# Kernel optimization log

Measured on AMD Instinct MI355X. Metric: run time of the kernel, lower is better.

The kernel has to match this reference:

```python
import jax, jax.numpy as jnp
from jax import lax
import numpy as np

B, S, T, R = 64, 50, 50, 2   # batch, n_prev_sents, n_words, n_responses
V, H = 32000, 256            # vocab, hidden (= emb_size)


def gru_scan(xs, h0, Wih, Whh, bih, bhh):
    """Torch-style GRU over xs [T, N, I]; returns (outs [T,N,H], h_last [N,H])."""
    gi_all = jnp.einsum('tni,gi->tng', xs, Wih) + bih  # input gates precomputed
    def step(h, gi):
        gh = h @ Whh.T + bhh
        ir, iz, inn = jnp.split(gi, 3, -1)
        hr, hz, hn = jnp.split(gh, 3, -1)
        r = jax.nn.sigmoid(ir + hr)
        z = jax.nn.sigmoid(iz + hz)
        n = jnp.tanh(inn + r * hn)
        h = (1.0 - z) * n + z * h
        return h, h
    h_last, outs = lax.scan(step, h0, gi_all)
    return outs, h_last


def agent_tables():
    # replicates get_agent_emb: np.random.seed(1), one fresh uniform table per batch
    np.random.seed(1)
    return jnp.asarray(np.stack([np.random.uniform(0, 1, (S + 1, H)) for _ in range(B)]).astype(np.float32))


def setup_inputs() -> dict:
    key = jax.random.key(0)
    ks = jax.random.split(key, 24)
    k = 1.0 / np.sqrt(H)
    u = lambda kk, shape: jax.random.uniform(kk, shape, jnp.float32, -k, k)
    inp = {
        'context': jax.random.randint(ks[0], (B, S, T), 0, V, jnp.int32),
        'response': jax.random.randint(ks[1], (B, R, T), 0, V, jnp.int32),
        'spk_agents': jax.random.randint(ks[2], (B, S), 0, S + 1, jnp.int32),
        'emb_utter': jax.random.normal(ks[3], (V, H), jnp.float32) * 0.1,
        'emb_resp': jax.random.normal(ks[4], (V, H), jnp.float32) * 0.1,
        'utter_Wih': u(ks[5], (3 * H, H)), 'utter_Whh': u(ks[6], (3 * H, H)),
        'utter_bih': u(ks[7], (3 * H,)), 'utter_bhh': u(ks[8], (3 * H,)),
        'ctx_Wih': u(ks[9], (3 * H, 2 * H)), 'ctx_Whh': u(ks[10], (3 * H, H)),
        'ctx_bih': u(ks[11], (3 * H,)), 'ctx_bhh': u(ks[12], (3 * H,)),
        'resp_Wih': u(ks[13], (3 * H, H)), 'resp_Whh': u(ks[14], (3 * H, H)),
        'resp_bih': u(ks[15], (3 * H,)), 'resp_bhh': u(ks[16], (3 * H,)),
        'spk_Wih': u(ks[17], (3 * H, H)), 'spk_Whh': u(ks[18], (3 * H, H)),
        'spk_bih': u(ks[19], (3 * H,)), 'spk_bhh': u(ks[20], (3 * H,)),
    }
    return inp


def forward(context, response, spk_agents, emb_utter, emb_resp,
            utter_Wih, utter_Whh, utter_bih, utter_bhh,
            ctx_Wih, ctx_Whh, ctx_bih, ctx_bhh,
            resp_Wih, resp_Whh, resp_bih, resp_bhh,
            spk_Wih, spk_Whh, spk_bih, spk_bhh):
    # ---- utterance encoder: all B*S utterances batched through one GRU ----
    xu = emb_utter[context.reshape(B * S, T)]                 # [B*S, T, H]
    xu = jnp.transpose(xu, (1, 0, 2))                         # [T, B*S, H]
    _, hu = gru_scan(xu, jnp.zeros((B * S, H), jnp.float32),
                     utter_Wih, utter_Whh, utter_bih, utter_bhh)
    utter_hidden = hu.reshape(B, S, H).transpose(1, 0, 2)     # [S, B, H]

    # ---- agent embeddings (per-batch random tables, gathered by speaker id) ----
    tables = agent_tables()                                   # [B, S+1, H] constant
    agent_emb = jnp.take_along_axis(tables, spk_agents[:, :, None].astype(jnp.int32), axis=1)  # [B,S,H]
    agent_emb = jnp.transpose(agent_emb, (1, 0, 2))           # [S, B, H]

    # ---- context GRU over utterances ----
    ctx_in = jnp.concatenate([utter_hidden, agent_emb], axis=2)  # [S, B, 2H]
    context_output, ctx_h = gru_scan(ctx_in, jnp.zeros((B, H), jnp.float32),
                                     ctx_Wih, ctx_Whh, ctx_bih, ctx_bhh)
    context_hidden = ctx_h[None]                              # [1, B, H]

    # ---- speaker encoder: masked GRU == GRU over each speaker's subsequence ----
    sp_ids = jnp.arange(S + 1)
    active = (spk_agents[:, :, None] == sp_ids[None, None, :])  # [B, S, S+1]
    active_t = jnp.transpose(active, (1, 0, 2))                 # [S, B, S+1]
    gi_all = jnp.einsum('sbh,gh->sbg', context_output, spk_Wih) + spk_bih  # [S, B, 3H]

    def spk_step(h, inputs):
        gi, act = inputs                                        # gi [B,3H], act [B,S+1]
        gh = jnp.einsum('bsh,gh->bsg', h, spk_Whh) + spk_bhh    # [B, S+1, 3H]
        ir, iz, inn = jnp.split(gi[:, None, :], 3, -1)
        hr, hz, hn = jnp.split(gh, 3, -1)
        r = jax.nn.sigmoid(ir + hr)
        z = jax.nn.sigmoid(iz + hz)
        n = jnp.tanh(inn + r * hn)
        h_new = (1.0 - z) * n + z * h
        return jnp.where(act[:, :, None], h_new, h), None

    h_spk, _ = lax.scan(spk_step, jnp.zeros((B, S + 1, H), jnp.float32), (gi_all, active_t))
    present = active.any(axis=1)                               # [B, S+1]
    spk_emb = h_spk * present[:, :, None]                      # rows of absent speakers stay 0
    spk_emb_mask = (present & (sp_ids[None, :] > 0)).astype(jnp.float32)  # [B, S+1]

    # ---- response encoder: all B*R responses batched ----
    xr = emb_resp[response.reshape(B * R, T)]                  # [B*R, T, H]
    xr = jnp.transpose(xr, (1, 0, 2))                          # [T, B*R, H]
    outs, hr_ = gru_scan(xr, jnp.zeros((B * R, H), jnp.float32),
                         resp_Wih, resp_Whh, resp_bih, resp_bhh)
    resp_output = outs.reshape(T, B, R, H).transpose(2, 0, 1, 3)  # [R, T, B, H]
    resp_hidden = hr_.reshape(B, R, H).transpose(1, 0, 2)         # [R, B, H]

    return (context_output, context_hidden, resp_output, resp_hidden, spk_emb, spk_emb_mask)


def reference(context, response, spk_agents, emb_utter, emb_resp,
              utter_Wih, utter_Whh, utter_bih, utter_bhh,
              ctx_Wih, ctx_Whh, ctx_bih, ctx_bhh,
              resp_Wih, resp_Whh, resp_bih, resp_bhh,
              spk_Wih, spk_Whh, spk_bih, spk_bhh):
    return forward(context, response, spk_agents, emb_utter, emb_resp,
                   utter_Wih, utter_Whh, utter_bih, utter_bhh,
                   ctx_Wih, ctx_Whh, ctx_bih, ctx_bhh,
                   resp_Wih, resp_Whh, resp_bih, resp_bhh,
                   spk_Wih, spk_Whh, spk_bih, spk_bhh)
```

## Files before the change

kernel.cpp:

```cpp
#include <hip/hip_runtime.h>
#include <hip/hip_bf16.h>
#include <stdint.h>
#include <stdlib.h>
#include <math.h>

typedef __hip_bfloat16 bf16;
typedef unsigned short ushort;
typedef __attribute__((ext_vector_type(8))) short bhalf8;
typedef __attribute__((ext_vector_type(4))) float f32x4;

#define Bn 64
#define Sn 50
#define Tn 50
#define Hn 256

#define OFF_CTX_OUT   0
#define OFF_CTX_HID   819200
#define OFF_RESP_OUT  835584
#define OFF_RESP_HID  2473984
#define OFF_SPK_EMB   2506752
#define OFF_SPK_MASK  3342336

#define WS_FLAG   0u
#define WS_HU     256u
#define WS_REG    1638912u
#define RG_UTTQ   0u
#define RG_UTTSC  24576000u
#define RG_RESPGI 0u
#define RG_CO     9830400u
#define RG_GIC    13107200u
#define RG_GIS    18022400u
#define RG_TBL    22937600u
#define WS_END    26342912u

__device__ __forceinline__ float b2f_bits(unsigned int b) {
    union { unsigned int u; float f; } c; c.u = b; return c.f;
}
__device__ __forceinline__ float bf2f(ushort v) { return b2f_bits(((unsigned int)v) << 16); }
__device__ __forceinline__ ushort f2bf(float f) {
    union { float f; unsigned int u; } c; c.f = f;
    return (ushort)((c.u + 0x7fffu + ((c.u >> 16) & 1u)) >> 16);
}
__device__ __forceinline__ void gld_lds16(const void* g, void* l) {
    __builtin_amdgcn_global_load_lds(
        (const __attribute__((address_space(1))) void*)g,
        (__attribute__((address_space(3))) void*)l, 16, 0, 0);
}
template<bool BF>
__device__ __forceinline__ bhalf8 ldfrag(const void* __restrict__ p, size_t i) {
    if (BF) {
        return *(const bhalf8*)((const ushort*)p + i);
    } else {
        const float* q = (const float*)p + i;
        float4 a = *(const float4*)q;
        float4 b = *(const float4*)(q + 4);
        bhalf8 r;
        r[0] = (short)f2bf(a.x); r[1] = (short)f2bf(a.y);
        r[2] = (short)f2bf(a.z); r[3] = (short)f2bf(a.w);
        r[4] = (short)f2bf(b.x); r[5] = (short)f2bf(b.y);
        r[6] = (short)f2bf(b.z); r[7] = (short)f2bf(b.w);
        return r;
    }
}
template<bool BF>
__device__ __forceinline__ float ldw(const void* __restrict__ p, int i) {
    return BF ? bf2f(((const ushort*)p)[i]) : ((const float*)p)[i];
}
template<bool BF>
__device__ __forceinline__ void stout(void* __restrict__ out, size_t i, float v) {
    if (BF) ((ushort*)out)[i] = f2bf(v);
    else    ((float*)out)[i] = v;
}
__device__ __forceinline__ float fsigm(float x) {
    return __builtin_amdgcn_rcpf(1.f + __expf(-x));
}
__device__ __forceinline__ float ftanh(float x) {
    float e = __expf(-2.f * x);
    return (1.f - e) * __builtin_amdgcn_rcpf(1.f + e);
}

__global__ void sniff_kernel(const void* __restrict__ w, int* __restrict__ flag) {
    const unsigned int* p = (const unsigned int*)w;
    int tid = threadIdx.x;
    bool big = false;
    for (int i = tid; i < 512; i += 64) {
        float v = b2f_bits(p[i] << 16);
        if (!(fabsf(v) <= 1.0f)) big = true;
    }
    unsigned long long m = __ballot(big);
    if (tid == 0) *flag = (m == 0ull) ? 1 : 0;
}


template<bool BF>
__device__ void vocab_utt_body(
    const void* __restrict__ emb_u, const void* __restrict__ uWih,
    const void* __restrict__ ubih,
    char* __restrict__ Q, float* __restrict__ SC,
    float* bhs, float (*rmx)[16])
{
    const int tid = threadIdx.x;
    const int w = tid >> 6, l = tid & 63, quad = l >> 4, c = l & 15;

    for (int i = tid; i < 768; i += 512) bhs[i] = ldw<BF>(ubih, i);

    bhalf8 wf[3][2][8];
    #pragma unroll
    for (int g = 0; g < 3; ++g)
        #pragma unroll
        for (int ctl = 0; ctl < 2; ++ctl) {
            const int gcol = g * 256 + 32 * w + 16 * ctl + c;
            #pragma unroll
            for (int tk = 0; tk < 8; ++tk)
                wf[g][ctl][tk] = ldfrag<BF>(uWih, (size_t)gcol * 256 + 32 * tk + 8 * quad);
        }
    __syncthreads();

    for (int vt = blockIdx.x; vt < 2000; vt += gridDim.x) {
        f32x4 acc[3][2];
        #pragma unroll
        for (int g = 0; g < 3; ++g)
            #pragma unroll
            for (int ctl = 0; ctl < 2; ++ctl) {
                float b = bhs[g * 256 + 32 * w + 16 * ctl + c];
                acc[g][ctl] = (f32x4){b, b, b, b};
            }
        #pragma unroll
        for (int tk = 0; tk < 8; ++tk) {
            bhalf8 a = ldfrag<BF>(emb_u, (size_t)(vt * 16 + c) * 256 + 32 * tk + 8 * quad);
            #pragma unroll
            for (int g = 0; g < 3; ++g)
                #pragma unroll
                for (int ctl = 0; ctl < 2; ++ctl)
                    acc[g][ctl] = __builtin_amdgcn_mfma_f32_16x16x32_bf16(
                        a, wf[g][ctl][tk], acc[g][ctl], 0, 0, 0);
        }

        float mx[4];
        #pragma unroll
        for (int r = 0; r < 4; ++r) {
            float v = 0.f;
            #pragma unroll
            for (int g = 0; g < 3; ++g)
                #pragma unroll
                for (int ctl = 0; ctl < 2; ++ctl)
                    v = fmaxf(v, fabsf(acc[g][ctl][r]));
            mx[r] = v;
        }
        #pragma unroll
        for (int off = 1; off < 16; off <<= 1)
            #pragma unroll
            for (int r = 0; r < 4; ++r)
                mx[r] = fmaxf(mx[r], __shfl_xor(mx[r], off));
        if (c == 0)
            #pragma unroll
            for (int r = 0; r < 4; ++r) rmx[w][4 * quad + r] = mx[r];
        __syncthreads();

        #pragma unroll
        for (int r = 0; r < 4; ++r) {
            const int m = 4 * quad + r;
            float s = fmaxf(fmaxf(fmaxf(rmx[0][m], rmx[1][m]), fmaxf(rmx[2][m], rmx[3][m])),
                            fmaxf(fmaxf(rmx[4][m], rmx[5][m]), fmaxf(rmx[6][m], rmx[7][m])));
            float scale = s * (1.f / 127.f);
            float inv   = (s > 0.f) ? (127.f / s) : 0.f;
            #pragma unroll
            for (int g = 0; g < 3; ++g)
                #pragma unroll
                for (int ctl = 0; ctl < 2; ++ctl) {
                    int qv = __float2int_rn(acc[g][ctl][r] * inv);
                    qv = max(-127, min(127, qv));
                    Q[(size_t)(vt * 16 + m) * 768 + g * 256 + 32 * w + 16 * ctl + c] = (char)qv;
                }
            if (w == 0 && c == 0) SC[vt * 16 + m] = scale;
        }
        __syncthreads();
    }
}

__global__ __launch_bounds__(512, 1) void vocab_utt_kernel(
    const void* emb_u, const void* uWih, const void* ubih,
    char* Q, float* SC, const int* flag)
{
    __shared__ float bhs[768];
    __shared__ float rmx[8][16];
    if (*flag) vocab_utt_body<true >(emb_u, uWih, ubih, Q, SC, bhs, rmx);
    else       vocab_utt_body<false>(emb_u, uWih, ubih, Q, SC, bhs, rmx);
}

template<bool BF>
__device__ void rec_utt_body(
    const int* __restrict__ ctx_tok,
    const char* __restrict__ Q, const float* __restrict__ SC,
    const void* __restrict__ uWhh, const void* __restrict__ ubhh,
    ushort* __restrict__ H_u,
    char (*gq)[16][784], float* gsc_all , ushort (*hb)[16][264])
{
    const int n0 = blockIdx.x * 16;
    const int tid = threadIdx.x;
    const int w = tid >> 6, l = tid & 63, quad = l >> 4, c = l & 15;

    for (int i = tid; i < 16 * 264; i += 512) (&hb[0][0][0])[i] = 0;
    for (int i = tid; i < Tn * 16; i += 512) {
        const int t = i >> 4, m = i & 15;
        gsc_all[i] = SC[ctx_tok[(n0 + m) * Tn + t]];
    }

    float breg[3][2];
    #pragma unroll
    for (int g = 0; g < 3; ++g)
        #pragma unroll
        for (int ctl = 0; ctl < 2; ++ctl)
            breg[g][ctl] = ldw<BF>(ubhh, g * 256 + 32 * w + 16 * ctl + c);

    bhalf8 wf[3][2][8];
    #pragma unroll
    for (int g = 0; g < 3; ++g)
        #pragma unroll
        for (int ctl = 0; ctl < 2; ++ctl) {
            const int gcol = g * 256 + 32 * w + 16 * ctl + c;
            #pragma unroll
            for (int tk = 0; tk < 8; ++tk)
                wf[g][ctl][tk] = ldfrag<BF>(uWhh, (size_t)gcol * 256 + 32 * tk + 8 * quad);
        }

    float st[2][4];
    #pragma unroll
    for (int ctl = 0; ctl < 2; ++ctl)
        #pragma unroll
        for (int r = 0; r < 4; ++r) st[ctl][r] = 0.f;

    #pragma unroll
    for (int k = 0; k < 2; ++k) {
        const int m = 2 * w + k;
        const int tok = ctx_tok[(n0 + m) * Tn + 0];
        if (l < 48)
            gld_lds16(Q + (size_t)tok * 768 + l * 16, &gq[0][m][0]);
    }
    __syncthreads();

    int p = 0;
    for (int t = 0; t < Tn; ++t) {
        if (t < Tn - 1) {
            #pragma unroll
            for (int k = 0; k < 2; ++k) {
                const int m = 2 * w + k;
                const int tok = ctx_tok[(n0 + m) * Tn + t + 1];
                if (l < 48)
                    gld_lds16(Q + (size_t)tok * 768 + l * 16, &gq[p ^ 1][m][0]);
            }
        }

        f32x4 acc[3][2];
        #pragma unroll
        for (int g = 0; g < 3; ++g)
            #pragma unroll
            for (int ctl = 0; ctl < 2; ++ctl) {
                float b = breg[g][ctl];
                acc[g][ctl] = (f32x4){b, b, b, b};
            }
        #pragma unroll
        for (int tk = 0; tk < 8; ++tk) {
            bhalf8 a = *(const bhalf8*)(&hb[p][c][32 * tk + 8 * quad]);
            #pragma unroll
            for (int g = 0; g < 3; ++g)
                #pragma unroll
                for (int ctl = 0; ctl < 2; ++ctl)
                    acc[g][ctl] = __builtin_amdgcn_mfma_f32_16x16x32_bf16(
                        a, wf[g][ctl][tk], acc[g][ctl], 0, 0, 0);
        }

        #pragma unroll
        for (int ctl = 0; ctl < 2; ++ctl) {
            const int u = 32 * w + 16 * ctl + c;
            #pragma unroll
            for (int r = 0; r < 4; ++r) {
                const int m = 4 * quad + r;
                const float s = gsc_all[t * 16 + m];
                float gr = s * (float)(signed char)gq[p][m][u];
                float gz = s * (float)(signed char)gq[p][m][256 + u];
                float gn = s * (float)(signed char)gq[p][m][512 + u];
                float rr = fsigm(gr + acc[0][ctl][r]);
                float zz = fsigm(gz + acc[1][ctl][r]);
                float nn = ftanh(gn + rr * acc[2][ctl][r]);
                float h  = (1.f - zz) * nn + zz * st[ctl][r];
                st[ctl][r] = h;
                hb[p ^ 1][m][u] = f2bf(h);
            }
        }
        __syncthreads();
        p ^= 1;
    }

    #pragma unroll
    for (int ctl = 0; ctl < 2; ++ctl)
        #pragma unroll
        for (int r = 0; r < 4; ++r)
            H_u[(size_t)(n0 + 4 * quad + r) * Hn + 32 * w + 16 * ctl + c] = f2bf(st[ctl][r]);
}

__global__ __launch_bounds__(512, 1) void rec_utt_kernel(
    const int* ctx_tok, const char* Q, const float* SC,
    const void* uWhh, const void* ubhh, ushort* H_u, const int* flag)
{
    __shared__ __align__(16) char   gq[2][16][784];
    __shared__ float  gsc_all[Tn * 16];
    __shared__ __align__(16) ushort hb[2][16][264];
    if (*flag) rec_utt_body<true >(ctx_tok, Q, SC, uWhh, ubhh, H_u, gq, gsc_all, hb);
    else       rec_utt_body<false>(ctx_tok, Q, SC, uWhh, ubhh, H_u, gq, gsc_all, hb);
}

template<bool BF>
__device__ void respgi_body(
    int bid,
    const int* __restrict__ rsp_tok, const void* __restrict__ emb_r,
    const void* __restrict__ rWih, const void* __restrict__ rbih,
    ushort* __restrict__ RG, float* bhs)
{
    const int tid = threadIdx.x;
    const int w = tid >> 6, l = tid & 63, quad = l >> 4, c = l & 15;

    for (int i = tid; i < 768; i += 512) bhs[i] = ldw<BF>(rbih, i);

    bhalf8 wf[3][2][8];
    #pragma unroll
    for (int g = 0; g < 3; ++g)
        #pragma unroll
        for (int ctl = 0; ctl < 2; ++ctl) {
            const int gcol = g * 256 + 32 * w + 16 * ctl + c;
            #pragma unroll
            for (int tk = 0; tk < 8; ++tk)
                wf[g][ctl][tk] = ldfrag<BF>(rWih, (size_t)gcol * 256 + 32 * tk + 8 * quad);
        }
    __syncthreads();

    const int inst = bid * 16 + c;
    const int tok  = rsp_tok[inst];

    f32x4 acc[3][2];
    #pragma unroll
    for (int g = 0; g < 3; ++g)
        #pragma unroll
        for (int ctl = 0; ctl < 2; ++ctl) {
            float b = bhs[g * 256 + 32 * w + 16 * ctl + c];
            acc[g][ctl] = (f32x4){b, b, b, b};
        }
    #pragma unroll
    for (int tk = 0; tk < 8; ++tk) {
        bhalf8 a = ldfrag<BF>(emb_r, (size_t)tok * 256 + 32 * tk + 8 * quad);
        #pragma unroll
        for (int g = 0; g < 3; ++g)
            #pragma unroll
            for (int ctl = 0; ctl < 2; ++ctl)
                acc[g][ctl] = __builtin_amdgcn_mfma_f32_16x16x32_bf16(
                    a, wf[g][ctl][tk], acc[g][ctl], 0, 0, 0);
    }
    #pragma unroll
    for (int g = 0; g < 3; ++g)
        #pragma unroll
        for (int ctl = 0; ctl < 2; ++ctl)
            #pragma unroll
            for (int r = 0; r < 4; ++r)
                RG[(size_t)(bid * 16 + 4 * quad + r) * 768
                   + g * 256 + 32 * w + 16 * ctl + c] = f2bf(acc[g][ctl][r]);
}

template<bool BF>
__device__ void rec_resp_body(
    int bid,
    const ushort* __restrict__ RG,
    const void* __restrict__ rWhh, const void* __restrict__ rbhh,
    void* __restrict__ outp,
    ushort (*gx)[16][776], ushort (*hb)[16][264])
{
    const int n0 = bid * 16;
    const int tid = threadIdx.x;
    const int w = tid >> 6, l = tid & 63, quad = l >> 4, c = l & 15;

    for (int i = tid; i < 16 * 264; i += 512) (&hb[0][0][0])[i] = 0;

    float breg[3][2];
    #pragma unroll
    for (int g = 0; g < 3; ++g)
        #pragma unroll
        for (int ctl = 0; ctl < 2; ++ctl)
            breg[g][ctl] = ldw<BF>(rbhh, g * 256 + 32 * w + 16 * ctl + c);

    bhalf8 wf[3][2][8];
    #pragma unroll
    for (int g = 0; g < 3; ++g)
        #pragma unroll
        for (int ctl = 0; ctl < 2; ++ctl) {
            const int gcol = g * 256 + 32 * w + 16 * ctl + c;
            #pragma unroll
            for (int tk = 0; tk < 8; ++tk)
                wf[g][ctl][tk] = ldfrag<BF>(rWhh, (size_t)gcol * 256 + 32 * tk + 8 * quad);
        }

    float st[2][4];
    #pragma unroll
    for (int ctl = 0; ctl < 2; ++ctl)
        #pragma unroll
        for (int r = 0; r < 4; ++r) st[ctl][r] = 0.f;

    #pragma unroll
    for (int k = 0; k < 2; ++k) {
        const int m = 2 * w + k;
        const ushort* src = RG + (size_t)((n0 + m) * Tn + 0) * 768;
        if (l < 48) {
            gld_lds16(src + l * 8,       &gx[0][m][0]);
            gld_lds16(src + 384 + l * 8, &gx[0][m][384]);
        }
    }
    __syncthreads();

    int p = 0;
    for (int t = 0; t < Tn; ++t) {
        if (t < Tn - 1) {
            #pragma unroll
            for (int k = 0; k < 2; ++k) {
                const int m = 2 * w + k;
                const ushort* src = RG + (size_t)((n0 + m) * Tn + t + 1) * 768;
                if (l < 48) {
                    gld_lds16(src + l * 8,       &gx[p ^ 1][m][0]);
                    gld_lds16(src + 384 + l * 8, &gx[p ^ 1][m][384]);
                }
            }
        }
        if (t > 0) {
            #pragma unroll
            for (int ctl = 0; ctl < 2; ++ctl) {
                const int u = 32 * w + 16 * ctl + c;
                #pragma unroll
                for (int r = 0; r < 4; ++r) {
                    const int n = n0 + 4 * quad + r, bb = n >> 1, ri = n & 1;
                    stout<BF>(outp, OFF_RESP_OUT
                              + (size_t)((ri * Tn + (t - 1)) * Bn + bb) * Hn + u,
                              st[ctl][r]);
                }
            }
        }

        f32x4 acc[3][2];
        #pragma unroll
        for (int g = 0; g < 3; ++g)
            #pragma unroll
            for (int ctl = 0; ctl < 2; ++ctl) {
                float b = breg[g][ctl];
                acc[g][ctl] = (f32x4){b, b, b, b};
            }
        #pragma unroll
        for (int tk = 0; tk < 8; ++tk) {
            bhalf8 a = *(const bhalf8*)(&hb[p][c][32 * tk + 8 * quad]);
            #pragma unroll
            for (int g = 0; g < 3; ++g)
                #pragma unroll
                for (int ctl = 0; ctl < 2; ++ctl)
                    acc[g][ctl] = __builtin_amdgcn_mfma_f32_16x16x32_bf16(
                        a, wf[g][ctl][tk], acc[g][ctl], 0, 0, 0);
        }

        #pragma unroll
        for (int ctl = 0; ctl < 2; ++ctl) {
            const int u = 32 * w + 16 * ctl + c;
            #pragma unroll
            for (int r = 0; r < 4; ++r) {
                const int m = 4 * quad + r;
                float gr = bf2f(gx[p][m][u]);
                float gz = bf2f(gx[p][m][256 + u]);
                float gn = bf2f(gx[p][m][512 + u]);
                float rr = fsigm(gr + acc[0][ctl][r]);
                float zz = fsigm(gz + acc[1][ctl][r]);
                float nn = ftanh(gn + rr * acc[2][ctl][r]);
                float h  = (1.f - zz) * nn + zz * st[ctl][r];
                st[ctl][r] = h;
                hb[p ^ 1][m][u] = f2bf(h);
            }
        }
        __syncthreads();
        p ^= 1;
    }

    #pragma unroll
    for (int ctl = 0; ctl < 2; ++ctl) {
        const int u = 32 * w + 16 * ctl + c;
        #pragma unroll
        for (int r = 0; r < 4; ++r) {
            const int n = n0 + 4 * quad + r, bb = n >> 1, ri = n & 1;
            stout<BF>(outp, OFF_RESP_OUT
                      + (size_t)((ri * Tn + (Tn - 1)) * Bn + bb) * Hn + u, st[ctl][r]);
            stout<BF>(outp, OFF_RESP_HID + (size_t)(ri * Bn + bb) * Hn + u, st[ctl][r]);
        }
    }
}

template<bool BF>
__device__ void gi_ctx_body(
    int bid,
    const ushort* __restrict__ H_u, const ushort* __restrict__ tblbf,
    const int* __restrict__ spk_agents,
    const void* __restrict__ Wih, const void* __restrict__ bih,
    ushort* __restrict__ GIc, float* bhs)
{
    const int tid = threadIdx.x;
    const int w = tid >> 6, l = tid & 63, quad = l >> 4, c = l & 15;

    for (int i = tid; i < 768; i += 512) bhs[i] = ldw<BF>(bih, i);
    __syncthreads();

    const int m0 = bid * 16;
    const int m  = m0 + c, s = m >> 6, b = m & 63;
    const int a  = spk_agents[b * Sn + s];
    const ushort* arow0 = H_u   + (size_t)(b * Sn + s) * Hn;
    const ushort* arow1 = tblbf + (size_t)(b * 51 + a) * Hn;

    f32x4 acc[3][2];
    #pragma unroll
    for (int g = 0; g < 3; ++g)
        #pragma unroll
        for (int ctl = 0; ctl < 2; ++ctl) {
            float bb = bhs[g * 256 + 32 * w + 16 * ctl + c];
            acc[g][ctl] = (f32x4){bb, bb, bb, bb};
        }

    for (int half = 0; half < 2; ++half) {
        const ushort* ar = half ? arow1 : arow0;
        bhalf8 af[8];
        #pragma unroll
        for (int tk = 0; tk < 8; ++tk)
            af[tk] = *(const bhalf8*)(ar + 32 * tk + 8 * quad);
        #pragma unroll
        for (int g = 0; g < 3; ++g) {
            bhalf8 wf[2][8];
            #pragma unroll
            for (int ctl = 0; ctl < 2; ++ctl) {
                const int gcol = g * 256 + 32 * w + 16 * ctl + c;
                #pragma unroll
                for (int tk = 0; tk < 8; ++tk)
                    wf[ctl][tk] = ldfrag<BF>(Wih,
                        (size_t)gcol * 512 + half * 256 + 32 * tk + 8 * quad);
            }
            #pragma unroll
            for (int tk = 0; tk < 8; ++tk)
                #pragma unroll
                for (int ctl = 0; ctl < 2; ++ctl)
                    acc[g][ctl] = __builtin_amdgcn_mfma_f32_16x16x32_bf16(
                        af[tk], wf[ctl][tk], acc[g][ctl], 0, 0, 0);
        }
    }

    #pragma unroll
    for (int g = 0; g < 3; ++g)
        #pragma unroll
        for (int ctl = 0; ctl < 2; ++ctl)
            #pragma unroll
            for (int r = 0; r < 4; ++r)
                GIc[(size_t)(m0 + 4 * quad + r) * 768
                    + g * 256 + 32 * w + 16 * ctl + c] = f2bf(acc[g][ctl][r]);
}

__global__ __launch_bounds__(512, 1) void gates2_kernel(
    const int* rsp_tok, const void* emb_r, const void* rWih, const void* rbih,
    ushort* RG,
    const ushort* H_u, const ushort* tblbf, const int* spk_agents,
    const void* cWih, const void* cbih, ushort* GIc, const int* flag)
{
    __shared__ float bhs[768];
    if (blockIdx.x < 400) {
        if (*flag) respgi_body<true >(blockIdx.x, rsp_tok, emb_r, rWih, rbih, RG, bhs);
        else       respgi_body<false>(blockIdx.x, rsp_tok, emb_r, rWih, rbih, RG, bhs);
    } else {
        const int bid = blockIdx.x - 400;
        if (*flag) gi_ctx_body<true >(bid, H_u, tblbf, spk_agents, cWih, cbih, GIc, bhs);
        else       gi_ctx_body<false>(bid, H_u, tblbf, spk_agents, cWih, cbih, GIc, bhs);
    }
}

template<bool BF>
__device__ void ctx_rec_body(
    int bid,
    const ushort* __restrict__ GIc,
    const void* __restrict__ Whh, const void* __restrict__ bhh,
    float* __restrict__ CO, void* __restrict__ outp,
    ushort (*gx)[16][776], ushort (*hb)[16][264])
{
    const int n0 = bid * 16;
    const int tid = threadIdx.x;
    const int w = tid >> 6, l = tid & 63, quad = l >> 4, c = l & 15;

    for (int i = tid; i < 16 * 264; i += 512) (&hb[0][0][0])[i] = 0;

    float breg[3][2];
    #pragma unroll
    for (int g = 0; g < 3; ++g)
        #pragma unroll
        for (int ctl = 0; ctl < 2; ++ctl)
            breg[g][ctl] = ldw<BF>(bhh, g * 256 + 32 * w + 16 * ctl + c);

    bhalf8 wf[3][2][8];
    #pragma unroll
    for (int g = 0; g < 3; ++g)
        #pragma unroll
        for (int ctl = 0; ctl < 2; ++ctl) {
            const int gcol = g * 256 + 32 * w + 16 * ctl + c;
            #pragma unroll
            for (int tk = 0; tk < 8; ++tk)
                wf[g][ctl][tk] = ldfrag<BF>(Whh, (size_t)gcol * 256 + 32 * tk + 8 * quad);
        }

    float st[2][4];
    #pragma unroll
    for (int ctl = 0; ctl < 2; ++ctl)
        #pragma unroll
        for (int r = 0; r < 4; ++r) st[ctl][r] = 0.f;

    #pragma unroll
    for (int k = 0; k < 2; ++k) {
        const int m = 2 * w + k;
        const ushort* src = GIc + (size_t)(0 * Bn + n0 + m) * 768;
        if (l < 48) {
            gld_lds16(src + l * 8,       &gx[0][m][0]);
            gld_lds16(src + 384 + l * 8, &gx[0][m][384]);
        }
    }
    __syncthreads();

    int p = 0;
    for (int t = 0; t < Sn; ++t) {
        if (t < Sn - 1) {
            #pragma unroll
            for (int k = 0; k < 2; ++k) {
                const int m = 2 * w + k;
                const ushort* src = GIc + (size_t)((t + 1) * Bn + n0 + m) * 768;
                if (l < 48) {
                    gld_lds16(src + l * 8,       &gx[p ^ 1][m][0]);
                    gld_lds16(src + 384 + l * 8, &gx[p ^ 1][m][384]);
                }
            }
        }
        if (t > 0) {
            #pragma unroll
            for (int ctl = 0; ctl < 2; ++ctl) {
                const int u = 32 * w + 16 * ctl + c;
                #pragma unroll
                for (int r = 0; r < 4; ++r) {
                    const size_t gri = (size_t)((t - 1) * Bn + n0 + 4 * quad + r);
                    CO[gri * Hn + u] = st[ctl][r];
                    stout<BF>(outp, OFF_CTX_OUT + gri * Hn + u, st[ctl][r]);
                }
            }
        }

        f32x4 acc[3][2];
        #pragma unroll
        for (int g = 0; g < 3; ++g)
            #pragma unroll
            for (int ctl = 0; ctl < 2; ++ctl) {
                float b = breg[g][ctl];
                acc[g][ctl] = (f32x4){b, b, b, b};
            }
        #pragma unroll
        for (int tk = 0; tk < 8; ++tk) {
            bhalf8 a = *(const bhalf8*)(&hb[p][c][32 * tk + 8 * quad]);
            #pragma unroll
            for (int g = 0; g < 3; ++g)
                #pragma unroll
                for (int ctl = 0; ctl < 2; ++ctl)
                    acc[g][ctl] = __builtin_amdgcn_mfma_f32_16x16x32_bf16(
                        a, wf[g][ctl][tk], acc[g][ctl], 0, 0, 0);
        }

        #pragma unroll
        for (int ctl = 0; ctl < 2; ++ctl) {
            const int u = 32 * w + 16 * ctl + c;
            #pragma unroll
            for (int r = 0; r < 4; ++r) {
                const int m = 4 * quad + r;
                float gr = bf2f(gx[p][m][u]);
                float gz = bf2f(gx[p][m][256 + u]);
                float gn = bf2f(gx[p][m][512 + u]);
                float rr = fsigm(gr + acc[0][ctl][r]);
                float zz = fsigm(gz + acc[1][ctl][r]);
                float nn = ftanh(gn + rr * acc[2][ctl][r]);
                float h  = (1.f - zz) * nn + zz * st[ctl][r];
                st[ctl][r] = h;
                hb[p ^ 1][m][u] = f2bf(h);
            }
        }
        __syncthreads();
        p ^= 1;
    }

    #pragma unroll
    for (int ctl = 0; ctl < 2; ++ctl) {
        const int u = 32 * w + 16 * ctl + c;
        #pragma unroll
        for (int r = 0; r < 4; ++r) {
            const int m = 4 * quad + r;
            const size_t gri = (size_t)((Sn - 1) * Bn + n0 + m);
            CO[gri * Hn + u] = st[ctl][r];
            stout<BF>(outp, OFF_CTX_OUT + gri * Hn + u, st[ctl][r]);
            stout<BF>(outp, OFF_CTX_HID + (size_t)(n0 + m) * Hn + u, st[ctl][r]);
        }
    }
}

__global__ __launch_bounds__(512, 1) void rec2_kernel(
    const ushort* GIc, const void* cWhh, const void* cbhh, float* CO,
    const ushort* RG, const void* rWhh, const void* rbhh,
    void* outp, const int* flag)
{
    __shared__ __align__(16) ushort gx[2][16][776];
    __shared__ __align__(16) ushort hb[2][16][264];
    if (blockIdx.x < 4) {
        if (*flag) ctx_rec_body<true >(blockIdx.x, GIc, cWhh, cbhh, CO, outp, gx, hb);
        else       ctx_rec_body<false>(blockIdx.x, GIc, cWhh, cbhh, CO, outp, gx, hb);
    } else {
        const int bid = blockIdx.x - 4;
        if (*flag) rec_resp_body<true >(bid, RG, rWhh, rbhh, outp, gx, hb);
        else       rec_resp_body<false>(bid, RG, rWhh, rbhh, outp, gx, hb);
    }
}

template<bool BF>
__device__ void gi_spk_body(
    const float* __restrict__ CO,
    const void* __restrict__ Wih, const void* __restrict__ bih,
    ushort* __restrict__ GIs, float* bhs)
{
    const int tid = threadIdx.x;
    const int w = tid >> 6, l = tid & 63, quad = l >> 4, c = l & 15;

    for (int i = tid; i < 768; i += 512) bhs[i] = ldw<BF>(bih, i);

    bhalf8 wf[3][2][8];
    #pragma unroll
    for (int g = 0; g < 3; ++g)
        #pragma unroll
        for (int ctl = 0; ctl < 2; ++ctl) {
            const int gcol = g * 256 + 32 * w + 16 * ctl + c;
            #pragma unroll
            for (int tk = 0; tk < 8; ++tk)
                wf[g][ctl][tk] = ldfrag<BF>(Wih, (size_t)gcol * 256 + 32 * tk + 8 * quad);
        }
    __syncthreads();

    f32x4 acc[3][2];
    #pragma unroll
    for (int g = 0; g < 3; ++g)
        #pragma unroll
        for (int ctl = 0; ctl < 2; ++ctl) {
            float b = bhs[g * 256 + 32 * w + 16 * ctl + c];
            acc[g][ctl] = (f32x4){b, b, b, b};
        }
    #pragma unroll
    for (int tk = 0; tk < 8; ++tk) {
        bhalf8 a = ldfrag<false>(CO, (size_t)(blockIdx.x * 16 + c) * 256 + 32 * tk + 8 * quad);
        #pragma unroll
        for (int g = 0; g < 3; ++g)
            #pragma unroll
            for (int ctl = 0; ctl < 2; ++ctl)
                acc[g][ctl] = __builtin_amdgcn_mfma_f32_16x16x32_bf16(
                    a, wf[g][ctl][tk], acc[g][ctl], 0, 0, 0);
    }
    #pragma unroll
    for (int g = 0; g < 3; ++g)
        #pragma unroll
        for (int ctl = 0; ctl < 2; ++ctl)
            #pragma unroll
            for (int r = 0; r < 4; ++r)
                GIs[(size_t)(blockIdx.x * 16 + 4 * quad + r) * 768
                    + g * 256 + 32 * w + 16 * ctl + c] = f2bf(acc[g][ctl][r]);
}

__global__ __launch_bounds__(512, 1) void gi_spk_kernel(
    const float* CO, const void* Wih, const void* bih, ushort* GIs, const int* flag)
{
    __shared__ float bhs[768];
    if (*flag) gi_spk_body<true >(CO, Wih, bih, GIs, bhs);
    else       gi_spk_body<false>(CO, Wih, bih, GIs, bhs);
}

#define SSTR 264
template<bool BF>
__device__ void spk_rec_body(
    const ushort* __restrict__ GIs,
    const void* __restrict__ Whh, const void* __restrict__ bhh,
    const int* __restrict__ spk_agents,
    void* __restrict__ outp,
    ushort* S , ushort (*gx)[4][776], int* pres , float* bhs)
{
    const int b0 = blockIdx.x * 4;
    const int tid = threadIdx.x;
    const int w = tid >> 6, l = tid & 63, quad = l >> 4, c = l & 15;

    for (int i = tid; i < 768; i += 512) bhs[i] = ldw<BF>(bhh, i);
    for (int i = tid; i < 4 * 51 * SSTR; i += 512) S[i] = 0;
    for (int i = tid; i < 4 * 51; i += 512) pres[i] = 0;

    bhalf8 wf[3][2][8];
    #pragma unroll
    for (int g = 0; g < 3; ++g)
        #pragma unroll
        for (int ctl = 0; ctl < 2; ++ctl) {
            const int gcol = g * 256 + 32 * w + 16 * ctl + c;
            #pragma unroll
            for (int tk = 0; tk < 8; ++tk)
                wf[g][ctl][tk] = ldfrag<BF>(Whh, (size_t)gcol * 256 + 32 * tk + 8 * quad);
        }

    {
        const int row = w >> 1, ch = w & 1;
        const ushort* src = GIs + (size_t)(0 * Bn + b0 + row) * 768 + ch * 384;
        if (l < 48) gld_lds16(src + l * 8, &gx[0][row][ch * 384]);
    }
    __syncthreads();

    int p = 0;
    for (int t = 0; t < Sn; ++t) {
        const int va = (c < 4) ? spk_agents[(b0 + c) * Sn + t] : 0;
        const int mb = (c < 4) ? c : 0;

        if (t < Sn - 1) {
            const int row = w >> 1, ch = w & 1;
            const ushort* src = GIs + (size_t)((t + 1) * Bn + b0 + row) * 768 + ch * 384;
            if (l < 48) gld_lds16(src + l * 8, &gx[p ^ 1][row][ch * 384]);
        }

        f32x4 acc[3][2];
        #pragma unroll
        for (int g = 0; g < 3; ++g)
            #pragma unroll
            for (int ctl = 0; ctl < 2; ++ctl) {
                float b = bhs[g * 256 + 32 * w + 16 * ctl + c];
                acc[g][ctl] = (f32x4){b, b, b, b};
            }
        const ushort* srow = &S[(mb * 51 + va) * SSTR];
        #pragma unroll
        for (int tk = 0; tk < 8; ++tk) {
            bhalf8 a = *(const bhalf8*)(srow + 32 * tk + 8 * quad);
            #pragma unroll
            for (int g = 0; g < 3; ++g)
                #pragma unroll
                for (int ctl = 0; ctl < 2; ++ctl)
                    acc[g][ctl] = __builtin_amdgcn_mfma_f32_16x16x32_bf16(
                        a, wf[g][ctl][tk], acc[g][ctl], 0, 0, 0);
        }
        __syncthreads();

        if (quad == 0) {
            int vv[4];
            #pragma unroll
            for (int r = 0; r < 4; ++r) vv[r] = spk_agents[(b0 + r) * Sn + t];
            #pragma unroll
            for (int ctl = 0; ctl < 2; ++ctl) {
                const int u = 32 * w + 16 * ctl + c;
                #pragma unroll
                for (int r = 0; r < 4; ++r) {
                    ushort* sp = &S[(r * 51 + vv[r]) * SSTR + u];
                    float gr = bf2f(gx[p][r][u]);
                    float gz = bf2f(gx[p][r][256 + u]);
                    float gn = bf2f(gx[p][r][512 + u]);
                    float hprev = bf2f(*sp);
                    float rr = fsigm(gr + acc[0][ctl][r]);
                    float zz = fsigm(gz + acc[1][ctl][r]);
                    float nn = ftanh(gn + rr * acc[2][ctl][r]);
                    float h  = (1.f - zz) * nn + zz * hprev;
                    *sp = f2bf(h);
                }
            }
        }
        if (tid < 4) pres[tid * 51 + spk_agents[(b0 + tid) * Sn + t]] = 1;
        __syncthreads();
        p ^= 1;
    }
    __syncthreads();

    for (int idx = tid; idx < 4 * 51 * 256; idx += 512) {
        const int mb2 = idx / (51 * 256);
        const int rem = idx - mb2 * (51 * 256);
        const int v = rem >> 8, u = rem & 255;
        float val = bf2f(S[(mb2 * 51 + v) * SSTR + u]);
        stout<BF>(outp, OFF_SPK_EMB + (size_t)((b0 + mb2) * 51 + v) * Hn + u, val);
    }
    for (int idx = tid; idx < 4 * 51; idx += 512) {
        const int mb2 = idx / 51, v = idx - mb2 * 51;
        stout<BF>(outp, OFF_SPK_MASK + (size_t)((b0 + mb2) * 51 + v),
                  (pres[mb2 * 51 + v] && v > 0) ? 1.f : 0.f);
    }
}

__global__ __launch_bounds__(512, 1) void spk_rec_kernel(
    const ushort* GIs, const void* Whh, const void* bhh,
    const int* spk_agents, void* outp, const int* flag)
{
    __shared__ __align__(16) ushort S[4 * 51 * SSTR];
    __shared__ __align__(16) ushort gx[2][4][776];
    __shared__ int    pres[4 * 51];
    __shared__ float  bhs[768];
    if (*flag) spk_rec_body<true >(GIs, Whh, bhh, spk_agents, outp, S, gx, pres, bhs);
    else       spk_rec_body<false>(GIs, Whh, bhh, spk_agents, outp, S, gx, pres, bhs);
}

namespace {
inline uint16_t host_f2bf(float f) {
    union { float f; uint32_t u; } c; c.f = f;
    return (uint16_t)((c.u + 0x7fffu + ((c.u >> 16) & 1u)) >> 16);
}
struct MT19937 {
    uint32_t mt[624]; int mti;
    void seed(uint32_t s) {
        mt[0] = s;
        for (int i = 1; i < 624; ++i)
            mt[i] = 1812433253u * (mt[i - 1] ^ (mt[i - 1] >> 30)) + (uint32_t)i;
        mti = 624;
    }
    uint32_t next() {
        if (mti >= 624) {
            for (int i = 0; i < 624; ++i) {
                uint32_t y = (mt[i] & 0x80000000u) | (mt[(i + 1) % 624] & 0x7fffffffu);
                mt[i] = mt[(i + 397) % 624] ^ (y >> 1) ^ ((y & 1u) ? 0x9908b0dfu : 0u);
            }
            mti = 0;
        }
        uint32_t y = mt[mti++];
        y ^= y >> 11; y ^= (y << 7) & 0x9d2c5680u; y ^= (y << 15) & 0xefc60000u; y ^= y >> 18;
        return y;
    }
    double rd() {
        uint32_t a = next() >> 5, b = next() >> 6;
        return (a * 67108864.0 + b) / 9007199254740992.0;
    }
};

uint16_t* get_host_tables() {
    static uint16_t* p = [] {
        void* q = nullptr;
        if (hipHostMalloc(&q, 835584 * sizeof(uint16_t), hipHostMallocDefault) != hipSuccess)
            q = malloc(835584 * sizeof(uint16_t));
        uint16_t* h = (uint16_t*)q;
        MT19937 g; g.seed(1u);
        for (int i = 0; i < 835584; ++i)
            h[i] = host_f2bf((float)g.rd());
        return h;
    }();
    return p;
}
}

extern "C" void kernel_launch(void* const* d_in, const int* in_sizes, int n_in,
                              void* d_out, int out_size, void* d_ws, size_t ws_size,
                              hipStream_t stream)
{
    const int* ctx_tok    = (const int*)d_in[0];
    const int* rsp_tok    = (const int*)d_in[1];
    const int* spk_agents = (const int*)d_in[2];
    const void* emb_u = d_in[3];
    const void* emb_r = d_in[4];
    const void* uWih = d_in[5],  *uWhh = d_in[6],  *ubih = d_in[7],  *ubhh = d_in[8];
    const void* cWih = d_in[9],  *cWhh = d_in[10], *cbih = d_in[11], *cbhh = d_in[12];
    const void* rWih = d_in[13], *rWhh = d_in[14], *rbih = d_in[15], *rbhh = d_in[16];
    const void* sWih = d_in[17], *sWhh = d_in[18], *sbih = d_in[19], *sbhh = d_in[20];
    (void)in_sizes; (void)n_in; (void)out_size; (void)ws_size;

    char* ws  = (char*)d_ws;
    char* reg = ws + WS_REG;
    int*      flag = (int*)(ws + WS_FLAG);
    ushort*   H_u  = (ushort*)(ws + WS_HU);
    char*     UQ   = (char*)(reg + RG_UTTQ);
    float*    USC  = (float*)(reg + RG_UTTSC);
    ushort*   RG   = (ushort*)(reg + RG_RESPGI);
    float*    CO   = (float*)(reg + RG_CO);
    ushort*   GIc  = (ushort*)(reg + RG_GIC);
    ushort*   GIs  = (ushort*)(reg + RG_GIS);
    ushort*   tbl  = (ushort*)(reg + RG_TBL);
    void*     out  = d_out;

    sniff_kernel<<<1, 64, 0, stream>>>(uWih, flag);

    vocab_utt_kernel<<<250, 512, 0, stream>>>(emb_u, uWih, ubih, UQ, USC, flag);
    rec_utt_kernel<<<200, 512, 0, stream>>>(ctx_tok, UQ, USC, uWhh, ubhh, H_u, flag);

    hipMemcpyAsync(tbl, get_host_tables(), 835584 * sizeof(uint16_t),
                   hipMemcpyHostToDevice, stream);

    gates2_kernel<<<600, 512, 0, stream>>>(rsp_tok, emb_r, rWih, rbih, RG,
                                           H_u, tbl, spk_agents, cWih, cbih, GIc, flag);

    rec2_kernel<<<12, 512, 0, stream>>>(GIc, cWhh, cbhh, CO,
                                        RG, rWhh, rbhh, out, flag);

    gi_spk_kernel<<<200, 512, 0, stream>>>(CO, sWih, sbih, GIs, flag);
    spk_rec_kernel<<<16, 512, 0, stream>>>(GIs, sWhh, sbhh, spk_agents, out, flag);
}
```

Before: 1.236 ms.

## Restructure speaker recurrence into independent per-agent chains across many blocks

Measured after the change: 1.158 ms. 1.07x faster.

```diff
diff --git a/kernel.cpp b/kernel.cpp
--- a/kernel.cpp
+++ b/kernel.cpp
@@ -31,7 +31,9 @@
 #define RG_GIC    13107200u
 #define RG_GIS    18022400u
 #define RG_TBL    22937600u
-#define WS_END    26342912u
+#define WS_EV     26342912u
+#define WS_CNT    26995712u
+#define WS_END    27008768u
 
 __device__ __forceinline__ float b2f_bits(unsigned int b) {
     union { unsigned int u; float f; } c; c.u = b; return c.f;
@@ -91,6 +93,20 @@
     if (tid == 0) *flag = (m == 0ull) ? 1 : 0;
 }
 
+__global__ void spk_prep_kernel(const int* __restrict__ spk,
+                                int* __restrict__ EV, int* __restrict__ CNT) {
+    const int b = threadIdx.x;
+    if (b >= Bn) return;
+    int cloc[51];
+    for (int v = 0; v < 51; ++v) cloc[v] = 0;
+    for (int t = 0; t < Sn; ++t) {
+        const int v = spk[b * Sn + t];
+        EV[(b * 51 + v) * Sn + cloc[v]] = t;
+        cloc[v]++;
+    }
+    for (int v = 0; v < 51; ++v) CNT[b * 51 + v] = cloc[v];
+}
+
 
 template<bool BF>
 __device__ void vocab_utt_body(
@@ -531,13 +547,13 @@
             af[tk] = *(const bhalf8*)(ar + 32 * tk + 8 * quad);
         #pragma unroll
         for (int g = 0; g < 3; ++g) {
-            bhalf8 wf[2][8];
+            bhalf8 wfl[2][8];
             #pragma unroll
             for (int ctl = 0; ctl < 2; ++ctl) {
                 const int gcol = g * 256 + 32 * w + 16 * ctl + c;
                 #pragma unroll
                 for (int tk = 0; tk < 8; ++tk)
-                    wf[ctl][tk] = ldfrag<BF>(Wih,
+                    wfl[ctl][tk] = ldfrag<BF>(Wih,
                         (size_t)gcol * 512 + half * 256 + 32 * tk + 8 * quad);
             }
             #pragma unroll
@@ -545,7 +561,7 @@
                 #pragma unroll
                 for (int ctl = 0; ctl < 2; ++ctl)
                     acc[g][ctl] = __builtin_amdgcn_mfma_f32_16x16x32_bf16(
-                        af[tk], wf[ctl][tk], acc[g][ctl], 0, 0, 0);
+                        af[tk], wfl[ctl][tk], acc[g][ctl], 0, 0, 0);
         }
     }
 
@@ -781,22 +797,27 @@
     else       gi_spk_body<false>(CO, Wih, bih, GIs, bhs);
 }
 
-#define SSTR 264
 template<bool BF>
-__device__ void spk_rec_body(
+__device__ void spk_chain_body(
     const ushort* __restrict__ GIs,
     const void* __restrict__ Whh, const void* __restrict__ bhh,
-    const int* __restrict__ spk_agents,
+    const int* __restrict__ EV, const int* __restrict__ CNT,
     void* __restrict__ outp,
-    ushort* S , ushort (*gx)[4][776], int* pres , float* bhs)
-{
-    const int b0 = blockIdx.x * 4;
+    ushort (*gx)[16][776], ushort (*hb)[16][264], int* cnts)
+{
+    const int ci0 = blockIdx.x * 16;
     const int tid = threadIdx.x;
     const int w = tid >> 6, l = tid & 63, quad = l >> 4, c = l & 15;
 
-    for (int i = tid; i < 768; i += 512) bhs[i] = ldw<BF>(bhh, i);
-    for (int i = tid; i < 4 * 51 * SSTR; i += 512) S[i] = 0;
-    for (int i = tid; i < 4 * 51; i += 512) pres[i] = 0;
+    for (int i = tid; i < 16 * 264; i += 512) (&hb[0][0][0])[i] = 0;
+    if (tid < 16) cnts[tid] = CNT[ci0 + tid];
+
+    float breg[3][2];
+    #pragma unroll
+    for (int g = 0; g < 3; ++g)
+        #pragma unroll
+        for (int ctl = 0; ctl < 2; ++ctl)
+            breg[g][ctl] = ldw<BF>(bhh, g * 256 + 32 * w + 16 * ctl + c);
 
     bhalf8 wf[3][2][8];
     #pragma unroll
@@ -809,97 +830,113 @@
                 wf[g][ctl][tk] = ldfrag<BF>(Whh, (size_t)gcol * 256 + 32 * tk + 8 * quad);
         }
 
-    {
-        const int row = w >> 1, ch = w & 1;
-        const ushort* src = GIs + (size_t)(0 * Bn + b0 + row) * 768 + ch * 384;
-        if (l < 48) gld_lds16(src + l * 8, &gx[0][row][ch * 384]);
-    }
+    float st[2][4];
+    #pragma unroll
+    for (int ctl = 0; ctl < 2; ++ctl)
+        #pragma unroll
+        for (int r = 0; r < 4; ++r) st[ctl][r] = 0.f;
+
     __syncthreads();
 
-    int p = 0;
-    for (int t = 0; t < Sn; ++t) {
-        const int va = (c < 4) ? spk_agents[(b0 + c) * Sn + t] : 0;
-        const int mb = (c < 4) ? c : 0;
-
-        if (t < Sn - 1) {
-            const int row = w >> 1, ch = w & 1;
-            const ushort* src = GIs + (size_t)((t + 1) * Bn + b0 + row) * 768 + ch * 384;
-            if (l < 48) gld_lds16(src + l * 8, &gx[p ^ 1][row][ch * 384]);
-        }
-
-        f32x4 acc[3][2];
-        #pragma unroll
-        for (int g = 0; g < 3; ++g)
-            #pragma unroll
-            for (int ctl = 0; ctl < 2; ++ctl) {
-                float b = bhs[g * 256 + 32 * w + 16 * ctl + c];
-                acc[g][ctl] = (f32x4){b, b, b, b};
-            }
-        const ushort* srow = &S[(mb * 51 + va) * SSTR];
-        #pragma unroll
-        for (int tk = 0; tk < 8; ++tk) {
-            bhalf8 a = *(const bhalf8*)(srow + 32 * tk + 8 * quad);
+    int Kmax = 0;
+    #pragma unroll
+    for (int m = 0; m < 16; ++m) Kmax = max(Kmax, cnts[m]);
+
+    if (Kmax > 0) {
+        #pragma unroll
+        for (int k0 = 0; k0 < 2; ++k0) {
+            const int m = 2 * w + k0, ci = ci0 + m, b = ci / 51;
+            const int te = (cnts[m] > 0) ? EV[ci * Sn + 0] : 0;
+            const ushort* src = GIs + (size_t)(te * Bn + b) * 768;
+            if (l < 48) {
+                gld_lds16(src + l * 8,       &gx[0][m][0]);
+                gld_lds16(src + 384 + l * 8, &gx[0][m][384]);
+            }
+        }
+        __syncthreads();
+
+        int p = 0;
+        for (int k = 0; k < Kmax; ++k) {
+            if (k < Kmax - 1) {
+                #pragma unroll
+                for (int k0 = 0; k0 < 2; ++k0) {
+                    const int m = 2 * w + k0, ci = ci0 + m, b = ci / 51;
+                    const int te = (k + 1 < cnts[m]) ? EV[ci * Sn + k + 1] : 0;
+                    const ushort* src = GIs + (size_t)(te * Bn + b) * 768;
+                    if (l < 48) {
+                        gld_lds16(src + l * 8,       &gx[p ^ 1][m][0]);
+                        gld_lds16(src + 384 + l * 8, &gx[p ^ 1][m][384]);
+                    }
+                }
+            }
+
+            f32x4 acc[3][2];
             #pragma unroll
             for (int g = 0; g < 3; ++g)
                 #pragma unroll
-                for (int ctl = 0; ctl < 2; ++ctl)
-                    acc[g][ctl] = __builtin_amdgcn_mfma_f32_16x16x32_bf16(
-                        a, wf[g][ctl][tk], acc[g][ctl], 0, 0, 0);
-        }
-        __syncthreads();
-
-        if (quad == 0) {
-            int vv[4];
-            #pragma unroll
-            for (int r = 0; r < 4; ++r) vv[r] = spk_agents[(b0 + r) * Sn + t];
+                for (int ctl = 0; ctl < 2; ++ctl) {
+                    float b = breg[g][ctl];
+                    acc[g][ctl] = (f32x4){b, b, b, b};
+                }
+            #pragma unroll
+            for (int tk = 0; tk < 8; ++tk) {
+                bhalf8 a = *(const bhalf8*)(&hb[p][c][32 * tk + 8 * quad]);
+                #pragma unroll
+                for (int g = 0; g < 3; ++g)
+                    #pragma unroll
+                    for (int ctl = 0; ctl < 2; ++ctl)
+                        acc[g][ctl] = __builtin_amdgcn_mfma_f32_16x16x32_bf16(
+                            a, wf[g][ctl][tk], acc[g][ctl], 0, 0, 0);
+            }
+
             #pragma unroll
             for (int ctl = 0; ctl < 2; ++ctl) {
                 const int u = 32 * w + 16 * ctl + c;
                 #pragma unroll
                 for (int r = 0; r < 4; ++r) {
-                    ushort* sp = &S[(r * 51 + vv[r]) * SSTR + u];
-                    float gr = bf2f(gx[p][r][u]);
-                    float gz = bf2f(gx[p][r][256 + u]);
-                    float gn = bf2f(gx[p][r][512 + u]);
-                    float hprev = bf2f(*sp);
+                    const int m = 4 * quad + r;
+                    const bool act = (k < cnts[m]);
+                    float gr = bf2f(gx[p][m][u]);
+                    float gz = bf2f(gx[p][m][256 + u]);
+                    float gn = bf2f(gx[p][m][512 + u]);
                     float rr = fsigm(gr + acc[0][ctl][r]);
                     float zz = fsigm(gz + acc[1][ctl][r]);
                     float nn = ftanh(gn + rr * acc[2][ctl][r]);
-                    float h  = (1.f - zz) * nn + zz * hprev;
-                    *sp = f2bf(h);
+                    float h  = (1.f - zz) * nn + zz * st[ctl][r];
+                    st[ctl][r] = act ? h : st[ctl][r];
+                    hb[p ^ 1][m][u] = f2bf(st[ctl][r]);
                 }
             }
-        }
-        if (tid < 4) pres[tid * 51 + spk_agents[(b0 + tid) * Sn + t]] = 1;
-        __syncthreads();
-        p ^= 1;
-    }
-    __syncthreads();
-
-    for (int idx = tid; idx < 4 * 51 * 256; idx += 512) {
-        const int mb2 = idx / (51 * 256);
-        const int rem = idx - mb2 * (51 * 256);
-        const int v = rem >> 8, u = rem & 255;
-        float val = bf2f(S[(mb2 * 51 + v) * SSTR + u]);
-        stout<BF>(outp, OFF_SPK_EMB + (size_t)((b0 + mb2) * 51 + v) * Hn + u, val);
-    }
-    for (int idx = tid; idx < 4 * 51; idx += 512) {
-        const int mb2 = idx / 51, v = idx - mb2 * 51;
-        stout<BF>(outp, OFF_SPK_MASK + (size_t)((b0 + mb2) * 51 + v),
-                  (pres[mb2 * 51 + v] && v > 0) ? 1.f : 0.f);
-    }
-}
-
-__global__ __launch_bounds__(512, 1) void spk_rec_kernel(
+            __syncthreads();
+            p ^= 1;
+        }
+    }
+
+    #pragma unroll
+    for (int ctl = 0; ctl < 2; ++ctl) {
+        const int u = 32 * w + 16 * ctl + c;
+        #pragma unroll
+        for (int r = 0; r < 4; ++r) {
+            const int ci = ci0 + 4 * quad + r;
+            stout<BF>(outp, OFF_SPK_EMB + (size_t)ci * Hn + u, st[ctl][r]);
+        }
+    }
+    if (tid < 16) {
+        const int ci = ci0 + tid, v = ci % 51;
+        stout<BF>(outp, OFF_SPK_MASK + (size_t)ci,
+                  (cnts[tid] > 0 && v > 0) ? 1.f : 0.f);
+    }
+}
+
+__global__ __launch_bounds__(512, 1) void spk_chain_kernel(
     const ushort* GIs, const void* Whh, const void* bhh,
-    const int* spk_agents, void* outp, const int* flag)
-{
-    __shared__ __align__(16) ushort S[4 * 51 * SSTR];
-    __shared__ __align__(16) ushort gx[2][4][776];
-    __shared__ int    pres[4 * 51];
-    __shared__ float  bhs[768];
-    if (*flag) spk_rec_body<true >(GIs, Whh, bhh, spk_agents, outp, S, gx, pres, bhs);
-    else       spk_rec_body<false>(GIs, Whh, bhh, spk_agents, outp, S, gx, pres, bhs);
+    const int* EV, const int* CNT, void* outp, const int* flag)
+{
+    __shared__ __align__(16) ushort gx[2][16][776];
+    __shared__ __align__(16) ushort hb[2][16][264];
+    __shared__ int cnts[16];
+    if (*flag) spk_chain_body<true >(GIs, Whh, bhh, EV, CNT, outp, gx, hb, cnts);
+    else       spk_chain_body<false>(GIs, Whh, bhh, EV, CNT, outp, gx, hb, cnts);
 }
 
 namespace {
@@ -974,9 +1011,12 @@
     ushort*   GIc  = (ushort*)(reg + RG_GIC);
     ushort*   GIs  = (ushort*)(reg + RG_GIS);
     ushort*   tbl  = (ushort*)(reg + RG_TBL);
+    int*      EV   = (int*)(ws + WS_EV);
+    int*      CNT  = (int*)(ws + WS_CNT);
     void*     out  = d_out;
 
     sniff_kernel<<<1, 64, 0, stream>>>(uWih, flag);
+    spk_prep_kernel<<<1, 64, 0, stream>>>(spk_agents, EV, CNT);
 
     vocab_utt_kernel<<<250, 512, 0, stream>>>(emb_u, uWih, ubih, UQ, USC, flag);
     rec_utt_kernel<<<200, 512, 0, stream>>>(ctx_tok, UQ, USC, uWhh, ubhh, H_u, flag);
@@ -991,5 +1031,5 @@
                                         RG, rWhh, rbhh, out, flag);
 
     gi_spk_kernel<<<200, 512, 0, stream>>>(CO, sWih, sbih, GIs, flag);
-    spk_rec_kernel<<<16, 512, 0, stream>>>(GIs, sWhh, sbhh, spk_agents, out, flag);
-}
+    spk_chain_kernel<<<204, 512, 0, stream>>>(GIs, sWhh, sbhh, EV, CNT, out, flag);
+}
```
